# Performance work log

Measured on AMD Instinct MI355X. Metric: run time of the kernel, lower is better.

The kernel has to match this reference:

```python
import jax, jax.numpy as jnp
import numpy as np

B = 4096
D_ACT = 768
D_HID = 24576
K = 32


def setup_inputs() -> dict:
    key = jax.random.key(0)
    kA, kW = jax.random.split(key)
    A = jax.random.normal(kA, (B, D_ACT), dtype=jnp.float32)
    # kaiming_uniform_(nonlinearity='relu') on a [d_act, d_hid] tensor:
    # torch fan_in = size(1) = d_hid, bound = sqrt(6 / fan_in)
    bound = float(np.sqrt(6.0 / D_HID))
    W_enc = jax.random.uniform(kW, (D_ACT, D_HID), dtype=jnp.float32,
                               minval=-bound, maxval=bound)
    W_dec = W_enc.T  # tied init: W_enc.data.mT
    b_pre = jnp.zeros((D_ACT,), dtype=jnp.float32)
    return {"A": A, "W_enc": W_enc, "W_dec": W_dec, "b_pre": b_pre, "k": K}


def reference(A, W_enc, W_dec, b_pre, k):
    # encode: (A - b_pre) @ W_enc -> [batch, d_hidden]
    acts = jnp.einsum('bd,dh->bh', A - b_pre, W_enc)
    # top-k over hidden dim (torch uses sorted=False; set of values is identical)
    top_acts, top_idx = jax.lax.top_k(acts, k)  # [batch, k] each
    # scatter the k active activations back into a dense z
    batch_idx = jnp.arange(acts.shape[0])[:, None]  # [batch, 1]
    z = jnp.zeros_like(acts).at[batch_idx, top_idx].set(top_acts)
    # decode: dense z @ W_dec + b_pre
    A_reconstruct = z @ W_dec + b_pre
    return (A_reconstruct, acts, z)
```

## Files before the change

kernel.cpp:

```cpp
#include <hip/hip_runtime.h>
#include <cstdint>

#define M_ROWS 4096
#define K_DIM  768
#define N_HID  24576
#define TOPK   32
#define MAXCAND 64
#define KC     2304

typedef float f32x4 __attribute__((ext_vector_type(4)));
typedef short s16x8 __attribute__((ext_vector_type(8)));

__device__ __forceinline__ unsigned short f2bf_rne(float f) {
    uint32_t u = __float_as_uint(f);
    uint32_t r = (u + 0x7fffu + ((u >> 16) & 1u)) >> 16;
    return (unsigned short)r;
}
__device__ __forceinline__ float bf2f(unsigned short h) {
    return __uint_as_float((uint32_t)h << 16);
}

#define GLOAD(g, l) __builtin_amdgcn_global_load_lds( \
    (const __attribute__((address_space(1))) uint32_t*)(g), \
    (__attribute__((address_space(3))) uint32_t*)(l), 16, 0, 0)

__global__ __launch_bounds__(256) void convert_a(
    const float* __restrict__ A, const float* __restrict__ b_pre,
    unsigned short* __restrict__ Acat)
{
    const int idx = blockIdx.x * 256 + threadIdx.x;
    const int m  = idx / (K_DIM / 4);
    const int k  = (idx % (K_DIM / 4)) * 4;
    const float4 a4 = *(const float4*)(A + (size_t)m * K_DIM + k);
    const float4 b4 = *(const float4*)(b_pre + k);
    const float av[4] = {a4.x - b4.x, a4.y - b4.y, a4.z - b4.z, a4.w - b4.w};
    unsigned short hi[4], lo[4];
    #pragma unroll
    for (int i = 0; i < 4; ++i) {
        hi[i] = f2bf_rne(av[i]);
        lo[i] = f2bf_rne(av[i] - bf2f(hi[i]));
    }
    unsigned short* row = Acat + (size_t)m * KC + k;
    *(ushort4*)(row)        = make_ushort4(hi[0], hi[1], hi[2], hi[3]);
    *(ushort4*)(row + 768)  = make_ushort4(hi[0], hi[1], hi[2], hi[3]);
    *(ushort4*)(row + 1536) = make_ushort4(lo[0], lo[1], lo[2], lo[3]);
}

__global__ __launch_bounds__(256) void convert_w(
    const float* __restrict__ W, unsigned short* __restrict__ WT)
{
    __shared__ float tile[64][65];
    const int tid = threadIdx.x;
    const int n0 = blockIdx.x * 64;
    const int k0 = blockIdx.y * 64;

    #pragma unroll
    for (int i = 0; i < 16; ++i) {
        int e = i * 256 + tid;
        int r = e >> 6, c = e & 63;
        tile[r][c] = W[(size_t)(k0 + r) * N_HID + n0 + c];
    }
    __syncthreads();
    #pragma unroll
    for (int i = 0; i < 8; ++i) {
        int p = i * 256 + tid;
        int n = p >> 5;
        int k2 = (p & 31) * 2;
        float v0 = tile[k2][n], v1 = tile[k2 + 1][n];
        unsigned short h0 = f2bf_rne(v0), h1 = f2bf_rne(v1);
        unsigned short l0 = f2bf_rne(v0 - bf2f(h0)), l1 = f2bf_rne(v1 - bf2f(h1));
        unsigned short* row = WT + (size_t)(n0 + n) * KC + k0 + k2;
        *(ushort2*)(row)        = make_ushort2(h0, h1);
        *(ushort2*)(row + 768)  = make_ushort2(l0, l1);
        *(ushort2*)(row + 1536) = make_ushort2(h0, h1);
    }
}

__global__ __launch_bounds__(256) void encode_mfma(
    const unsigned short* __restrict__ Acat, const unsigned short* __restrict__ WT,
    float* __restrict__ acts)
{
    __shared__ unsigned short As[128 * 32];
    __shared__ unsigned short Bs[128 * 32];

    const int tid  = threadIdx.x;
    const int lane = tid & 63;
    const int wave = tid >> 6;
    const int wr = wave >> 1;
    const int wc = wave & 1;
    const int m0 = blockIdx.y * 128;
    const int n0 = blockIdx.x * 128;

    f32x4 acc[4][4] = {};

    const int c0   = wave * 2;
    const int row0 = c0 * 16 + (lane >> 2);
    const int kel  = (lane & 3) * 8;
    const unsigned short* aSrc0 = Acat + (size_t)(m0 + row0) * KC + kel;
    const unsigned short* aSrc1 = aSrc0 + (size_t)16 * KC;
    const unsigned short* bSrc0 = WT   + (size_t)(n0 + row0) * KC + kel;
    const unsigned short* bSrc1 = bSrc0 + (size_t)16 * KC;
    unsigned short* aDst0 = As + c0 * 512;
    unsigned short* aDst1 = As + (c0 + 1) * 512;
    unsigned short* bDst0 = Bs + c0 * 512;
    unsigned short* bDst1 = Bs + (c0 + 1) * 512;

    const int aoff = (wr * 64 + (lane & 15)) * 32 + (lane >> 4) * 8;
    const int boff = (wc * 64 + (lane & 15)) * 32 + (lane >> 4) * 8;

    for (int k0 = 0; k0 < KC; k0 += 32) {
        GLOAD(aSrc0 + k0, aDst0);
        GLOAD(aSrc1 + k0, aDst1);
        GLOAD(bSrc0 + k0, bDst0);
        GLOAD(bSrc1 + k0, bDst1);
        __syncthreads();

        s16x8 a[4], b[4];
        #pragma unroll
        for (int i = 0; i < 4; ++i)
            a[i] = *(const s16x8*)(As + aoff + i * 16 * 32);
        #pragma unroll
        for (int j = 0; j < 4; ++j)
            b[j] = *(const s16x8*)(Bs + boff + j * 16 * 32);
        #pragma unroll
        for (int i = 0; i < 4; ++i)
            #pragma unroll
            for (int j = 0; j < 4; ++j)
                asm("v_mfma_f32_16x16x32_bf16 %0, %1, %2, %0"
                    : "+v"(acc[i][j]) : "v"(a[i]), "v"(b[j]));
        __syncthreads();
    }

    const int crow = (lane >> 4) * 4;
    const int ccol = lane & 15;
    #pragma unroll
    for (int i = 0; i < 4; ++i) {
        #pragma unroll
        for (int r = 0; r < 4; ++r) {
            float* dst = acts + (size_t)(m0 + wr * 64 + i * 16 + crow + r) * N_HID
                       + n0 + wc * 64 + ccol;
            #pragma unroll
            for (int j = 0; j < 4; ++j)
                dst[j * 16] = acc[i][j][r];
        }
    }
}

__device__ __forceinline__ uint32_t f2k(float f) {
    uint32_t b = __float_as_uint(f);
    return (b & 0x80000000u) ? ~b : (b | 0x80000000u);
}
__device__ __forceinline__ float k2f(uint32_t k) {
    return __uint_as_float((k & 0x80000000u) ? (k ^ 0x80000000u) : ~k);
}

__global__ __launch_bounds__(256) void topk_decode(
    const float* __restrict__ acts, const float* __restrict__ A,
    const float* __restrict__ W_dec, const float* __restrict__ b_pre,
    float* __restrict__ z, float* __restrict__ recon)
{
    const int row = blockIdx.x;
    const int tid = threadIdx.x;
    const float* arow = acts + (size_t)row * N_HID;

    __shared__ float    ash[K_DIM];
    __shared__ uint32_t hist[256];
    __shared__ uint32_t sfx[256];
    __shared__ uint32_t bsel, bgt;
    __shared__ int      candN;
    __shared__ int      candIdx[MAXCAND];
    __shared__ double   candVal[MAXCAND];
    __shared__ double   partsum[4][MAXCAND];
    __shared__ int      selIdx[TOPK];
    __shared__ float    selVal[TOPK];

    for (int i = tid; i < K_DIM; i += 256) ash[i] = A[(size_t)row * K_DIM + i] - b_pre[i];

    uint32_t key[96];
    #pragma unroll
    for (int i = 0; i < 24; ++i) {
        const float4 v = *(const float4*)(arow + ((size_t)(tid + i * 256) << 2));
        key[i * 4 + 0] = f2k(v.x);
        key[i * 4 + 1] = f2k(v.y);
        key[i * 4 + 2] = f2k(v.z);
        key[i * 4 + 3] = f2k(v.w);
    }

    uint32_t prefix = 0;
    uint32_t kneed = TOPK;
    for (int shift = 24; shift >= 0; shift -= 8) {
        hist[tid] = 0u;
        __syncthreads();
        #pragma unroll
        for (int i = 0; i < 96; ++i) {
            uint32_t kk = key[i];
            bool m = (shift == 24) || ((kk >> (shift + 8)) == prefix);
            if (m) atomicAdd(&hist[(kk >> shift) & 255u], 1u);
        }
        __syncthreads();
        sfx[tid] = hist[tid];
        __syncthreads();
        for (int off = 1; off < 256; off <<= 1) {
            uint32_t t = (tid + off < 256) ? sfx[tid + off] : 0u;
            __syncthreads();
            sfx[tid] += t;
            __syncthreads();
        }
        uint32_t ge = sfx[tid];
        uint32_t gt = (tid < 255) ? sfx[tid + 1] : 0u;
        if (gt < kneed && kneed <= ge) { bsel = (uint32_t)tid; bgt = gt; }
        __syncthreads();
        prefix = (prefix << 8) | bsel;
        kneed -= bgt;
        __syncthreads();
    }
    const float vT = k2f(prefix);
    const uint32_t keyLo = f2k(vT - 1e-3f);

    if (tid == 0) candN = 0;
    __syncthreads();
    #pragma unroll
    for (int i = 0; i < 24; ++i) {
        #pragma unroll
        for (int j = 0; j < 4; ++j) {
            if (key[i * 4 + j] >= keyLo) {
                int s = atomicAdd(&candN, 1);
                if (s < MAXCAND) candIdx[s] = (tid + i * 256) * 4 + j;
            }
        }
    }
    __syncthreads();
    const int nc = candN < MAXCAND ? candN : MAXCAND;

    {
        const int c = tid & 63, part = tid >> 6;
        double s = 0.0;
        if (c < nc) {
            const float* wr = W_dec + (size_t)candIdx[c] * K_DIM + part * 192;
            const float* ar = ash + part * 192;
            #pragma unroll 4
            for (int d = 0; d < 192; ++d) s += (double)ar[d] * (double)wr[d];
        }
        partsum[part][c] = s;
    }
    __syncthreads();
    if (tid < MAXCAND)
        candVal[tid] = partsum[0][tid] + partsum[1][tid] + partsum[2][tid] + partsum[3][tid];
    __syncthreads();

    if (tid < nc) {
        const double v = candVal[tid];
        const int    idx = candIdx[tid];
        int rank = 0;
        for (int t = 0; t < nc; ++t) {
            double vt2 = candVal[t]; int it = candIdx[t];
            if (vt2 > v || (vt2 == v && it < idx)) rank++;
        }
        if (rank < TOPK) { selIdx[rank] = idx; selVal[rank] = (float)v; }
    }
    __syncthreads();

    float* zrow = z + (size_t)row * N_HID;
    const float4 zero4 = make_float4(0.f, 0.f, 0.f, 0.f);
    #pragma unroll
    for (int i = 0; i < 24; ++i)
        *(float4*)(zrow + ((size_t)(tid + i * 256) << 2)) = zero4;
    __syncthreads();
    if (tid < TOPK) zrow[selIdx[tid]] = selVal[tid];

    const int d0 = tid;
    float a0 = b_pre[d0], a1 = b_pre[d0 + 256], a2 = b_pre[d0 + 512];
    #pragma unroll 8
    for (int s = 0; s < TOPK; ++s) {
        const float v = selVal[s];
        const float* wr = W_dec + (size_t)selIdx[s] * K_DIM;
        a0 = fmaf(v, wr[d0], a0);
        a1 = fmaf(v, wr[d0 + 256], a1);
        a2 = fmaf(v, wr[d0 + 512], a2);
    }
    float* rrow = recon + (size_t)row * K_DIM;
    rrow[d0] = a0;
    rrow[d0 + 256] = a1;
    rrow[d0 + 512] = a2;
}

extern "C" void kernel_launch(void* const* d_in, const int* in_sizes, int n_in,
                              void* d_out, int out_size, void* d_ws, size_t ws_size,
                              hipStream_t stream) {
    const float* A     = (const float*)d_in[0];
    const float* W_enc = (const float*)d_in[1];
    const float* W_dec = (const float*)d_in[2];
    const float* b_pre = (const float*)d_in[3];

    float* recon = (float*)d_out;
    float* acts  = recon + (size_t)M_ROWS * K_DIM;
    float* zbuf  = acts + (size_t)M_ROWS * N_HID;

    unsigned short* WT   = (unsigned short*)zbuf;
    unsigned short* Acat = WT + (size_t)N_HID * KC;

    convert_a<<<M_ROWS * K_DIM / 4 / 256, 256, 0, stream>>>(A, b_pre, Acat);
    convert_w<<<dim3(N_HID / 64, K_DIM / 64), 256, 0, stream>>>(W_enc, WT);
    encode_mfma<<<dim3(N_HID / 128, M_ROWS / 128), 256, 0, stream>>>(Acat, WT, acts);
    topk_decode<<<M_ROWS, 256, 0, stream>>>(acts, A, W_dec, b_pre, zbuf, recon);
}
```

Baseline: 1.728 ms.

## Replace 4-pass radix top-k select with single 4096-bin histogram pass

The top-k threshold search drops the four 8-bit radix passes, each with a histogram and a 256-wide scan, and does one 12-bit histogram over the top key bits with a per-thread 16-bin local scan plus one block scan. Because the threshold is now coarse, the candidate buffer grows to 128 and the double-precision exact rescoring is split into two halves with two accumulators. This removes many barriers and atomic passes, but more candidates may land in the coarse bin. If more than 128 values fall above the lowered threshold, some true top-k entries could be dropped.

```diff
diff --git a/kernel.cpp b/kernel.cpp
--- a/kernel.cpp
+++ b/kernel.cpp
@@ -5,8 +5,8 @@
 #define K_DIM  768
 #define N_HID  24576
 #define TOPK   32
-#define MAXCAND 64
-#define KC     2304
+#define MAXCAND 128
+#define NBIN   4096
 
 typedef float f32x4 __attribute__((ext_vector_type(4)));
 typedef short s16x8 __attribute__((ext_vector_type(8)));
@@ -23,6 +23,8 @@
 #define GLOAD(g, l) __builtin_amdgcn_global_load_lds( \
     (const __attribute__((address_space(1))) uint32_t*)(g), \
     (__attribute__((address_space(3))) uint32_t*)(l), 16, 0, 0)
+
+#define KC 2304
 
 __global__ __launch_bounds__(256) void convert_a(
     const float* __restrict__ A, const float* __restrict__ b_pre,
@@ -164,17 +166,21 @@
     const float* arow = acts + (size_t)row * N_HID;
 
     __shared__ float    ash[K_DIM];
-    __shared__ uint32_t hist[256];
+    __shared__ uint32_t hist[NBIN];
     __shared__ uint32_t sfx[256];
-    __shared__ uint32_t bsel, bgt;
+    __shared__ uint32_t bsel;
     __shared__ int      candN;
     __shared__ int      candIdx[MAXCAND];
     __shared__ double   candVal[MAXCAND];
-    __shared__ double   partsum[4][MAXCAND];
+    __shared__ double   partsum[2][MAXCAND];
     __shared__ int      selIdx[TOPK];
     __shared__ float    selVal[TOPK];
 
     for (int i = tid; i < K_DIM; i += 256) ash[i] = A[(size_t)row * K_DIM + i] - b_pre[i];
+
+    #pragma unroll
+    for (int i = 0; i < NBIN / 256; ++i) hist[tid + i * 256] = 0u;
+    if (tid == 0) candN = 0;
 
     uint32_t key[96];
     #pragma unroll
@@ -185,40 +191,41 @@
         key[i * 4 + 2] = f2k(v.z);
         key[i * 4 + 3] = f2k(v.w);
     }
-
-    uint32_t prefix = 0;
-    uint32_t kneed = TOPK;
-    for (int shift = 24; shift >= 0; shift -= 8) {
-        hist[tid] = 0u;
+    __syncthreads();
+
+    #pragma unroll
+    for (int i = 0; i < 96; ++i) atomicAdd(&hist[key[i] >> 20], 1u);
+    __syncthreads();
+
+    uint32_t loc[16];
+    {
+        uint32_t run = 0;
+        #pragma unroll
+        for (int j = 15; j >= 0; --j) { run += hist[tid * 16 + j]; loc[j] = run; }
+        sfx[tid] = run;
+    }
+    __syncthreads();
+    for (int off = 1; off < 256; off <<= 1) {
+        uint32_t t = (tid + off < 256) ? sfx[tid + off] : 0u;
         __syncthreads();
-        #pragma unroll
-        for (int i = 0; i < 96; ++i) {
-            uint32_t kk = key[i];
-            bool m = (shift == 24) || ((kk >> (shift + 8)) == prefix);
-            if (m) atomicAdd(&hist[(kk >> shift) & 255u], 1u);
-        }
+        sfx[tid] += t;
         __syncthreads();
-        sfx[tid] = hist[tid];
-        __syncthreads();
-        for (int off = 1; off < 256; off <<= 1) {
-            uint32_t t = (tid + off < 256) ? sfx[tid + off] : 0u;
-            __syncthreads();
-            sfx[tid] += t;
-            __syncthreads();
-        }
-        uint32_t ge = sfx[tid];
-        uint32_t gt = (tid < 255) ? sfx[tid + 1] : 0u;
-        if (gt < kneed && kneed <= ge) { bsel = (uint32_t)tid; bgt = gt; }
-        __syncthreads();
-        prefix = (prefix << 8) | bsel;
-        kneed -= bgt;
-        __syncthreads();
-    }
-    const float vT = k2f(prefix);
+    }
+    {
+        const uint32_t S_before = (tid < 255) ? sfx[tid + 1] : 0u;
+        uint32_t Sb1 = S_before;
+        #pragma unroll
+        for (int j = 15; j >= 0; --j) {
+            uint32_t Sb = S_before + loc[j];
+            if (Sb >= TOPK && Sb1 < TOPK) bsel = (uint32_t)(tid * 16 + j);
+            Sb1 = Sb;
+        }
+    }
+    __syncthreads();
+
+    const float vT = k2f(bsel << 20);
     const uint32_t keyLo = f2k(vT - 1e-3f);
 
-    if (tid == 0) candN = 0;
-    __syncthreads();
     #pragma unroll
     for (int i = 0; i < 24; ++i) {
         #pragma unroll
@@ -233,19 +240,22 @@
     const int nc = candN < MAXCAND ? candN : MAXCAND;
 
     {
-        const int c = tid & 63, part = tid >> 6;
-        double s = 0.0;
+        const int c = tid & 127, part = tid >> 7;
+        double s0 = 0.0, s1 = 0.0;
         if (c < nc) {
-            const float* wr = W_dec + (size_t)candIdx[c] * K_DIM + part * 192;
-            const float* ar = ash + part * 192;
+            const float* wr = W_dec + (size_t)candIdx[c] * K_DIM + part * 384;
+            const float* ar = ash + part * 384;
             #pragma unroll 4
-            for (int d = 0; d < 192; ++d) s += (double)ar[d] * (double)wr[d];
-        }
-        partsum[part][c] = s;
+            for (int d = 0; d < 384; d += 2) {
+                s0 += (double)ar[d]     * (double)wr[d];
+                s1 += (double)ar[d + 1] * (double)wr[d + 1];
+            }
+        }
+        partsum[part][c] = s0 + s1;
     }
     __syncthreads();
     if (tid < MAXCAND)
-        candVal[tid] = partsum[0][tid] + partsum[1][tid] + partsum[2][tid] + partsum[3][tid];
+        candVal[tid] = partsum[0][tid] + partsum[1][tid];
     __syncthreads();
 
     if (tid < nc) {
```

Result: faster. 1.671 ms (-3.3%).
